# Performance work log

Hardware: AMD Instinct MI355X
Metric: run time of the kernel (lower is better)

## Reference

```python
import jax, jax.numpy as jnp
import numpy as np

N_EMBD = 512
NUM_HEADS = 8
HEAD_SIZE = 64


def setup_inputs() -> dict:
    key = jax.random.key(0)
    ks = jax.random.split(key, 6)
    B, T, C, H, D = 64, 256, N_EMBD, NUM_HEADS, HEAD_SIZE
    s = 0.02
    return {
        "x": jax.random.normal(ks[0], (B, T, C), dtype=jnp.float32),
        "wq": jax.random.normal(ks[1], (H, C, D), dtype=jnp.float32) * s,
        "wk": jax.random.normal(ks[2], (H, C, D), dtype=jnp.float32) * s,
        "wv": jax.random.normal(ks[3], (H, C, D), dtype=jnp.float32) * s,
        "bq": jnp.zeros((H, D), dtype=jnp.float32),
        "bk": jnp.zeros((H, D), dtype=jnp.float32),
        "bv": jnp.zeros((H, D), dtype=jnp.float32),
        "wo": jax.random.normal(ks[4], (H * D, C), dtype=jnp.float32) * s,
        "bo": jnp.zeros((C,), dtype=jnp.float32),
    }


def reference(x, wq, wk, wv, bq, bk, bv, wo, bo):
    B, T, C = x.shape
    H, _, D = wq.shape
    # per-head QKV projections (vectorized over heads)
    q = jnp.einsum('btc,hcd->bhtd', x, wq) + bq[None, :, None, :]
    k = jnp.einsum('btc,hcd->bhtd', x, wk) + bk[None, :, None, :]
    v = jnp.einsum('btc,hcd->bhtd', x, wv) + bv[None, :, None, :]
    scale = 1.0 / jnp.sqrt(jnp.asarray(D, dtype=x.dtype))
    scores = jnp.einsum('bhtd,bhsd->bhts', q, k) * scale  # [B,H,T,T]
    causal = jnp.tril(jnp.ones((T, T), dtype=bool))
    scores = jnp.where(causal[None, None], scores, -jnp.inf)
    weights = jax.nn.softmax(scores, axis=-1)  # dropout omitted (eval mode)
    out = jnp.einsum('bhts,bhsd->bhtd', weights, v)  # [B,H,T,D]
    combined = out.transpose(0, 2, 1, 3).reshape(B, T, H * D)
    return combined @ wo + bo
```

## Files before the change

kernel.cpp:

```cpp
#include <hip/hip_runtime.h>

typedef unsigned int   u32;
typedef unsigned short u16;
typedef __attribute__((ext_vector_type(8))) short short8;
typedef __attribute__((ext_vector_type(4))) float f32x4;


__device__ __forceinline__ u16 f2bf(float f) {
    u32 u = __float_as_uint(f);
    u += 0x7fffu + ((u >> 16) & 1u);
    return (u16)(u >> 16);
}

__device__ __forceinline__ void gload_lds16(const u16* g, u16* l) {
    __builtin_amdgcn_global_load_lds(
        (const __attribute__((address_space(1))) u32*)(const void*)g,
        (__attribute__((address_space(3))) u32*)(void*)l, 16, 0, 0);
}

__global__ void cast_x_kernel(const float* __restrict__ x, u16* __restrict__ xb) {
    int i = blockIdx.x * 256 + threadIdx.x;
    float4 v = ((const float4*)x)[i];
    ushort4 o;
    o.x = f2bf(v.x); o.y = f2bf(v.y); o.z = f2bf(v.z); o.w = f2bf(v.w);
    ((ushort4*)xb)[i] = o;
}

__global__ void pack_wqkv_kernel(const float* __restrict__ wq, const float* __restrict__ wk,
                                 const float* __restrict__ wv, u16* __restrict__ wt) {
    int i = blockIdx.x * 256 + threadIdx.x;
    int n = i >> 9, c = i & 511;
    int proj = n >> 9, hd = n & 511;
    int h = hd >> 6, d = hd & 63;
    const float* w = (proj == 0) ? wq : (proj == 1) ? wk : wv;
    wt[(size_t)n * 512 + c] = f2bf(w[h * 32768 + c * 64 + d]);
}

__global__ void pack_wo_kernel(const float* __restrict__ wo, u16* __restrict__ wt) {
    int i = blockIdx.x * 256 + threadIdx.x;
    int n = i >> 9, k = i & 511;
    wt[(size_t)n * 512 + k] = f2bf(wo[(size_t)k * 512 + n]);
}

template<int EPI, int NT>
__global__ __launch_bounds__(256)
void gemm128_kernel(const u16* __restrict__ A, const u16* __restrict__ Bt,
                    float* __restrict__ outf, const float* __restrict__ bo,
                    u16* __restrict__ Qb, u16* __restrict__ Kb, u16* __restrict__ Vb,
                    const float* __restrict__ bq, const float* __restrict__ bk,
                    const float* __restrict__ bv) {
    __shared__ __align__(16) u16 As[2][8192];
    __shared__ __align__(16) u16 Bs[2][8192];
    const int tid = threadIdx.x;
    const int bid = blockIdx.x;
    const int xcd = bid & 7;
    const int k8  = bid >> 3;
    const int m0 = (xcd * 16 + k8 / NT) * 128;
    const int n0 = (k8 % NT) * 128;
    const int w = tid >> 6, lane = tid & 63;
    const int srow = w * 8 + (lane >> 3);
    const int sc   = (lane & 7) ^ ((lane >> 3) & 7);
    const u16* Ag = A  + (size_t)(m0 + srow) * 512 + sc * 8;
    const u16* Bg = Bt + (size_t)(n0 + srow) * 512 + sc * 8;
    const int lofs = w * 512 + lane * 8;

    const int wrow = (w >> 1) * 64, wcol = (w & 1) * 64;
    const int lm = lane & 15, quad = lane >> 4;
    const int l7 = lm & 7;

    f32x4 acc[4][4] = {};

    #pragma unroll
    for (int j = 0; j < 4; ++j) {
        gload_lds16(Ag + j * (32 * 512), As[0] + j * 2048 + lofs);
        gload_lds16(Bg + j * (32 * 512), Bs[0] + j * 2048 + lofs);
    }

    #pragma unroll 1
    for (int kt = 0; kt < 8; ++kt) {
        __syncthreads();
        if (kt < 7) {
            const u16* Agp = Ag + (kt + 1) * 64;
            const u16* Bgp = Bg + (kt + 1) * 64;
            u16* Asp = As[(kt + 1) & 1] + lofs;
            u16* Bsp = Bs[(kt + 1) & 1] + lofs;
            #pragma unroll
            for (int j = 0; j < 4; ++j) {
                gload_lds16(Agp + j * (32 * 512), Asp + j * 2048);
                gload_lds16(Bgp + j * (32 * 512), Bsp + j * 2048);
            }
        }
        const u16* Ac = As[kt & 1];
        const u16* Bc = Bs[kt & 1];
        short8 af[2][4], bf[2][4];
        #pragma unroll
        for (int h = 0; h < 2; ++h) {
            const int slot = ((h * 4 + quad) ^ l7) * 8;
            #pragma unroll
            for (int mi = 0; mi < 4; ++mi)
                af[h][mi] = *(const short8*)(Ac + (wrow + mi * 16 + lm) * 64 + slot);
            #pragma unroll
            for (int ni = 0; ni < 4; ++ni)
                bf[h][ni] = *(const short8*)(Bc + (wcol + ni * 16 + lm) * 64 + slot);
        }
        #pragma unroll
        for (int h = 0; h < 2; ++h)
            #pragma unroll
            for (int mi = 0; mi < 4; ++mi)
                #pragma unroll
                for (int ni = 0; ni < 4; ++ni)
                    acc[mi][ni] = __builtin_amdgcn_mfma_f32_16x16x32_bf16(af[h][mi], bf[h][ni], acc[mi][ni], 0, 0, 0);
    }

    if (EPI == 1) {
        #pragma unroll
        for (int ni = 0; ni < 4; ++ni) {
            int ncol = n0 + wcol + ni * 16 + lm;
            float bias = bo[ncol];
            #pragma unroll
            for (int mi = 0; mi < 4; ++mi) {
                int mbase = m0 + wrow + mi * 16 + quad * 4;
                #pragma unroll
                for (int r = 0; r < 4; ++r)
                    outf[(size_t)(mbase + r) * 512 + ncol] = acc[mi][ni][r] + bias;
            }
        }
    } else {
        #pragma unroll
        for (int ni = 0; ni < 4; ++ni) {
            int ncol = n0 + wcol + ni * 16 + lm;
            int proj = ncol >> 9, hd = ncol & 511;
            int h = hd >> 6, d = hd & 63;
            const float* bptr = (proj == 0) ? bq : (proj == 1) ? bk : bv;
            u16* dst = (proj == 0) ? Qb : (proj == 1) ? Kb : Vb;
            float bias = bptr[hd];
            #pragma unroll
            for (int mi = 0; mi < 4; ++mi) {
                int mbase = m0 + wrow + mi * 16 + quad * 4;
                #pragma unroll
                for (int r = 0; r < 4; ++r) {
                    int mrow = mbase + r;
                    int b = mrow >> 8, t = mrow & 255;
                    size_t idx = (proj == 2)
                        ? ((size_t)((b * 8 + h) * 64 + d) * 256 + t)
                        : ((size_t)((b * 8 + h) * 256 + t) * 64 + d);
                    dst[idx] = f2bf(acc[mi][ni][r] + bias);
                }
            }
        }
    }
}

__global__ __launch_bounds__(256)
void attn_mfma_kernel(const u16* __restrict__ Qg, const u16* __restrict__ Kg,
                      const u16* __restrict__ Vtg, u16* __restrict__ attn) {
    __shared__ __align__(16) u16 lds[20480];
    const int bid = blockIdx.x;
    const int head = (bid & 7) * 64 + ((bid >> 3) >> 1);
    const int iset = (bid >> 3) & 1;
    const int b = head >> 3, h = head & 7;
    const int tid = threadIdx.x;
    const size_t hb = (size_t)head * 16384;

    {
        const uint4* Ksrc = (const uint4*)(Kg + hb);
        uint4* L4 = (uint4*)lds;
        #pragma unroll
        for (int it = 0; it < 8; ++it) {
            int g = it * 256 + tid;
            int kr = g >> 3, kc = g & 7;
            L4[kr * 8 + (kc ^ (kr & 7))] = Ksrc[g];
        }
    }
    __syncthreads();

    const int w = tid >> 6, lane = tid & 63;
    const int lm = lane & 15, quad = lane >> 4;
    const int l7 = lm & 7;

    const int kx0 = (quad ^ l7) * 8;
    const int kx1 = ((4 + quad) ^ l7) * 8;
    const u16* Kbase = lds + lm * 64;
    const u16* Vg = Vtg + hb;
    const int Pbase = 16384 + w * 1024;
    const int x0 = (lm >> 3) & 1;
    const int pw_even = Pbase + quad * 16 + l7 + x0 * 8;
    const int pw_odd  = Pbase + quad * 16 + l7 + (x0 ^ 1) * 8;
    const int pr0 = Pbase + ((lm & 3) * 4 + (quad >> 1)) * 64
                  + (2 * (lm >> 2) + ((quad & 1) ^ (lm & 1))) * 8;

    #pragma unroll 1
    for (int ii = 0; ii < 2; ++ii) {
        const int i = iset ? (ii ? 2 : 1) : (ii ? 3 : 0);
        const int t0 = i * 64 + w * 16;
        short8 qa0 = *(const short8*)(Qg + hb + (size_t)(t0 + lm) * 64 + quad * 8);
        short8 qa1 = *(const short8*)(Qg + hb + (size_t)(t0 + lm) * 64 + 32 + quad * 8);
        f32x4 O[4] = {};
        float mr[4] = {-INFINITY, -INFINITY, -INFINITY, -INFINITY};
        float lr[4] = {0.f, 0.f, 0.f, 0.f};

        #pragma unroll 1
        for (int j = 0; j <= i; ++j) {
            f32x4 S[4] = {};
            #pragma unroll
            for (int ni = 0; ni < 4; ++ni) {
                const u16* kp = Kbase + j * 4096 + ni * 1024;
                short8 kb0 = *(const short8*)(kp + kx0);
                short8 kb1 = *(const short8*)(kp + kx1);
                S[ni] = __builtin_amdgcn_mfma_f32_16x16x32_bf16(qa0, kb0, S[ni], 0, 0, 0);
                S[ni] = __builtin_amdgcn_mfma_f32_16x16x32_bf16(qa1, kb1, S[ni], 0, 0, 0);
            }
            short8 vb[4][2];
            #pragma unroll
            for (int nd = 0; nd < 4; ++nd) {
                const u16* vp = Vg + (size_t)(nd * 16 + lm) * 256 + j * 64;
                vb[nd][0] = *(const short8*)(vp + quad * 8);
                vb[nd][1] = *(const short8*)(vp + 32 + quad * 8);
            }
            if (j == i) {
                #pragma unroll
                for (int ni = 0; ni < 4; ++ni) {
                    int scol = ni * 16 + lm;
                    #pragma unroll
                    for (int rr = 0; rr < 4; ++rr) {
                        int tloc = w * 16 + quad * 4 + rr;
                        S[ni][rr] = (scol > tloc) ? -INFINITY : S[ni][rr] * 0.125f;
                    }
                }
            } else {
                #pragma unroll
                for (int ni = 0; ni < 4; ++ni)
                    #pragma unroll
                    for (int rr = 0; rr < 4; ++rr)
                        S[ni][rr] *= 0.125f;
            }
            float alpha[4];
            #pragma unroll
            for (int rr = 0; rr < 4; ++rr) {
                float mx = fmaxf(fmaxf(S[0][rr], S[1][rr]), fmaxf(S[2][rr], S[3][rr]));
                mx = fmaxf(mx, __shfl_xor(mx, 1));
                mx = fmaxf(mx, __shfl_xor(mx, 2));
                mx = fmaxf(mx, __shfl_xor(mx, 4));
                mx = fmaxf(mx, __shfl_xor(mx, 8));
                float mnew = fmaxf(mr[rr], mx);
                alpha[rr] = __expf(mr[rr] - mnew);
                mr[rr] = mnew;
            }
            float rs[4] = {0.f, 0.f, 0.f, 0.f};
            #pragma unroll
            for (int ni = 0; ni < 4; ++ni) {
                #pragma unroll
                for (int rr = 0; rr < 4; ++rr) {
                    float p = __expf(S[ni][rr] - mr[rr]);
                    rs[rr] += p;
                    int addr = ((rr & 1) ? pw_odd : pw_even) + (rr * 4 + ni) * 64;
                    lds[addr] = f2bf(p);
                }
            }
            #pragma unroll
            for (int rr = 0; rr < 4; ++rr) {
                float s = rs[rr];
                s += __shfl_xor(s, 1);
                s += __shfl_xor(s, 2);
                s += __shfl_xor(s, 4);
                s += __shfl_xor(s, 8);
                lr[rr] = lr[rr] * alpha[rr] + s;
                O[0][rr] *= alpha[rr]; O[1][rr] *= alpha[rr];
                O[2][rr] *= alpha[rr]; O[3][rr] *= alpha[rr];
            }
            __syncthreads();
            short8 pa0 = *(const short8*)(lds + pr0);
            short8 pa1 = *(const short8*)(lds + pr0 + 128);
            #pragma unroll
            for (int nd = 0; nd < 4; ++nd) {
                O[nd] = __builtin_amdgcn_mfma_f32_16x16x32_bf16(pa0, vb[nd][0], O[nd], 0, 0, 0);
                O[nd] = __builtin_amdgcn_mfma_f32_16x16x32_bf16(pa1, vb[nd][1], O[nd], 0, 0, 0);
            }
        }
        #pragma unroll
        for (int rr = 0; rr < 4; ++rr) {
            float inv = 1.0f / lr[rr];
            int t = t0 + quad * 4 + rr;
            u16* op = attn + (size_t)(b * 256 + t) * 512 + h * 64 + lm;
            op[0]  = f2bf(O[0][rr] * inv);
            op[16] = f2bf(O[1][rr] * inv);
            op[32] = f2bf(O[2][rr] * inv);
            op[48] = f2bf(O[3][rr] * inv);
        }
    }
}

extern "C" void kernel_launch(void* const* d_in, const int* in_sizes, int n_in,
                              void* d_out, int out_size, void* d_ws, size_t ws_size,
                              hipStream_t stream) {
    const float* x  = (const float*)d_in[0];
    const float* wq = (const float*)d_in[1];
    const float* wk = (const float*)d_in[2];
    const float* wv = (const float*)d_in[3];
    const float* bq = (const float*)d_in[4];
    const float* bk = (const float*)d_in[5];
    const float* bv = (const float*)d_in[6];
    const float* wo = (const float*)d_in[7];
    const float* bo = (const float*)d_in[8];
    float* out = (float*)d_out;

    char* ws = (char*)d_ws;
    const size_t SZ = 16777216;
    u16* xb    = (u16*)(ws);
    u16* Qb    = (u16*)(ws + SZ);
    u16* Kb    = (u16*)(ws + 2 * SZ);
    u16* Vt    = (u16*)(ws + 3 * SZ);
    u16* attn  = (u16*)(ws + 4 * SZ);
    u16* wqkvT = (u16*)(ws + 5 * SZ);
    u16* woT   = (u16*)(ws + 5 * SZ + 1572864);

    cast_x_kernel<<<8192, 256, 0, stream>>>(x, xb);
    pack_wqkv_kernel<<<3072, 256, 0, stream>>>(wq, wk, wv, wqkvT);
    pack_wo_kernel<<<1024, 256, 0, stream>>>(wo, woT);

    gemm128_kernel<0, 12><<<1536, 256, 0, stream>>>(
        xb, wqkvT, nullptr, nullptr, Qb, Kb, Vt, bq, bk, bv);

    attn_mfma_kernel<<<1024, 256, 0, stream>>>(Qb, Kb, Vt, attn);

    gemm128_kernel<1, 4><<<512, 256, 0, stream>>>(
        attn, woT, out, bo, nullptr, nullptr, nullptr, nullptr, nullptr, nullptr);
}
```

Baseline: 205.6 us.

## Use 512-thread GEMM blocks with triple-buffered LDS and vmcnt-based prefetch

Result: slower. 223.3 us (+8.6%).

```diff
diff --git a/kernel.cpp b/kernel.cpp
--- a/kernel.cpp
+++ b/kernel.cpp
@@ -43,14 +43,14 @@
 }
 
 template<int EPI, int NT>
-__global__ __launch_bounds__(256)
+__global__ __launch_bounds__(512)
 void gemm128_kernel(const u16* __restrict__ A, const u16* __restrict__ Bt,
                     float* __restrict__ outf, const float* __restrict__ bo,
                     u16* __restrict__ Qb, u16* __restrict__ Kb, u16* __restrict__ Vb,
                     const float* __restrict__ bq, const float* __restrict__ bk,
                     const float* __restrict__ bv) {
-    __shared__ __align__(16) u16 As[2][8192];
-    __shared__ __align__(16) u16 Bs[2][8192];
+    __shared__ __align__(16) u16 As[3][8192];
+    __shared__ __align__(16) u16 Bs[3][8192];
     const int tid = threadIdx.x;
     const int bid = blockIdx.x;
     const int xcd = bid & 7;
@@ -62,37 +62,41 @@
     const int sc   = (lane & 7) ^ ((lane >> 3) & 7);
     const u16* Ag = A  + (size_t)(m0 + srow) * 512 + sc * 8;
     const u16* Bg = Bt + (size_t)(n0 + srow) * 512 + sc * 8;
-    const int lofs = w * 512 + lane * 8;
-
-    const int wrow = (w >> 1) * 64, wcol = (w & 1) * 64;
+    const int lofs = tid * 8;
+
+    const int wrow = (w >> 2) * 64, wcol = (w & 3) * 32;
     const int lm = lane & 15, quad = lane >> 4;
     const int l7 = lm & 7;
 
-    f32x4 acc[4][4] = {};
-
-    #pragma unroll
-    for (int j = 0; j < 4; ++j) {
-        gload_lds16(Ag + j * (32 * 512), As[0] + j * 2048 + lofs);
-        gload_lds16(Bg + j * (32 * 512), Bs[0] + j * 2048 + lofs);
-    }
-
+    f32x4 acc[4][2] = {};
+
+#define STAGE(kt, b) do {                                        \
+        const u16* Agp = Ag + (kt) * 64;                         \
+        const u16* Bgp = Bg + (kt) * 64;                         \
+        u16* Asp = As[(b)] + lofs;                               \
+        u16* Bsp = Bs[(b)] + lofs;                               \
+        gload_lds16(Agp,            Asp);                        \
+        gload_lds16(Agp + 64 * 512, Asp + 4096);                 \
+        gload_lds16(Bgp,            Bsp);                        \
+        gload_lds16(Bgp + 64 * 512, Bsp + 4096);                 \
+    } while (0)
+
+    STAGE(0, 0);
+    STAGE(1, 1);
+
+    int cur = 0;
     #pragma unroll 1
     for (int kt = 0; kt < 8; ++kt) {
-        __syncthreads();
-        if (kt < 7) {
-            const u16* Agp = Ag + (kt + 1) * 64;
-            const u16* Bgp = Bg + (kt + 1) * 64;
-            u16* Asp = As[(kt + 1) & 1] + lofs;
-            u16* Bsp = Bs[(kt + 1) & 1] + lofs;
-            #pragma unroll
-            for (int j = 0; j < 4; ++j) {
-                gload_lds16(Agp + j * (32 * 512), Asp + j * 2048);
-                gload_lds16(Bgp + j * (32 * 512), Bsp + j * 2048);
-            }
-        }
-        const u16* Ac = As[kt & 1];
-        const u16* Bc = Bs[kt & 1];
-        short8 af[2][4], bf[2][4];
+        if (kt < 7) asm volatile("s_waitcnt vmcnt(4)" ::: "memory");
+        else        asm volatile("s_waitcnt vmcnt(0)" ::: "memory");
+        __builtin_amdgcn_s_barrier();
+        if (kt < 6) {
+            int sb = cur ? cur - 1 : 2;
+            STAGE(kt + 2, sb);
+        }
+        const u16* Ac = As[cur];
+        const u16* Bc = Bs[cur];
+        short8 af[2][4], bf[2][2];
         #pragma unroll
         for (int h = 0; h < 2; ++h) {
             const int slot = ((h * 4 + quad) ^ l7) * 8;
@@ -100,7 +104,7 @@
             for (int mi = 0; mi < 4; ++mi)
                 af[h][mi] = *(const short8*)(Ac + (wrow + mi * 16 + lm) * 64 + slot);
             #pragma unroll
-            for (int ni = 0; ni < 4; ++ni)
+            for (int ni = 0; ni < 2; ++ni)
                 bf[h][ni] = *(const short8*)(Bc + (wcol + ni * 16 + lm) * 64 + slot);
         }
         #pragma unroll
@@ -108,13 +112,15 @@
             #pragma unroll
             for (int mi = 0; mi < 4; ++mi)
                 #pragma unroll
-                for (int ni = 0; ni < 4; ++ni)
+                for (int ni = 0; ni < 2; ++ni)
                     acc[mi][ni] = __builtin_amdgcn_mfma_f32_16x16x32_bf16(af[h][mi], bf[h][ni], acc[mi][ni], 0, 0, 0);
+        cur = (cur == 2) ? 0 : cur + 1;
     }
+#undef STAGE
 
     if (EPI == 1) {
         #pragma unroll
-        for (int ni = 0; ni < 4; ++ni) {
+        for (int ni = 0; ni < 2; ++ni) {
             int ncol = n0 + wcol + ni * 16 + lm;
             float bias = bo[ncol];
             #pragma unroll
@@ -127,7 +133,7 @@
         }
     } else {
         #pragma unroll
-        for (int ni = 0; ni < 4; ++ni) {
+        for (int ni = 0; ni < 2; ++ni) {
             int ncol = n0 + wcol + ni * 16 + lm;
             int proj = ncol >> 9, hd = ncol & 511;
             int h = hd >> 6, d = hd & 63;
@@ -318,11 +324,11 @@
     pack_wqkv_kernel<<<3072, 256, 0, stream>>>(wq, wk, wv, wqkvT);
     pack_wo_kernel<<<1024, 256, 0, stream>>>(wo, woT);
 
-    gemm128_kernel<0, 12><<<1536, 256, 0, stream>>>(
+    gemm128_kernel<0, 12><<<1536, 512, 0, stream>>>(
         xb, wqkvT, nullptr, nullptr, Qb, Kb, Vt, bq, bk, bv);
 
     attn_mfma_kernel<<<1024, 256, 0, stream>>>(Qb, Kb, Vt, attn);
 
-    gemm128_kernel<1, 4><<<512, 256, 0, stream>>>(
+    gemm128_kernel<1, 4><<<512, 512, 0, stream>>>(
         attn, woT, out, bo, nullptr, nullptr, nullptr, nullptr, nullptr, nullptr);
 }
```

## Replace LDS-tiled GEMM with B-panel-resident kernel streaming A from global

Applied to the files above, without the earlier changes.

New measurement: 238.7 us. 1.16x slower.

```diff
diff --git a/kernel.cpp b/kernel.cpp
--- a/kernel.cpp
+++ b/kernel.cpp
@@ -43,70 +43,54 @@
 }
 
 template<int EPI, int NT>
-__global__ __launch_bounds__(256)
-void gemm128_kernel(const u16* __restrict__ A, const u16* __restrict__ Bt,
-                    float* __restrict__ outf, const float* __restrict__ bo,
-                    u16* __restrict__ Qb, u16* __restrict__ Kb, u16* __restrict__ Vb,
-                    const float* __restrict__ bq, const float* __restrict__ bk,
-                    const float* __restrict__ bv) {
-    __shared__ __align__(16) u16 As[2][8192];
-    __shared__ __align__(16) u16 Bs[2][8192];
+__global__ __launch_bounds__(1024)
+void gemm_bpanel_kernel(const u16* __restrict__ A, const u16* __restrict__ Bt,
+                        float* __restrict__ outf, const float* __restrict__ bo,
+                        u16* __restrict__ Qb, u16* __restrict__ Kb, u16* __restrict__ Vb,
+                        const float* __restrict__ bq, const float* __restrict__ bk,
+                        const float* __restrict__ bv) {
+    __shared__ __align__(16) u16 Bp[64 * 512];
     const int tid = threadIdx.x;
     const int bid = blockIdx.x;
     const int xcd = bid & 7;
-    const int k8  = bid >> 3;
-    const int m0 = (xcd * 16 + k8 / NT) * 128;
-    const int n0 = (k8 % NT) * 128;
+    const int idx = bid >> 3;
+    const int m0 = (xcd * 4 + idx / NT) * 512;
+    const int nt = idx % NT;
+    const int n0 = nt * 64;
     const int w = tid >> 6, lane = tid & 63;
-    const int srow = w * 8 + (lane >> 3);
-    const int sc   = (lane & 7) ^ ((lane >> 3) & 7);
-    const u16* Ag = A  + (size_t)(m0 + srow) * 512 + sc * 8;
-    const u16* Bg = Bt + (size_t)(n0 + srow) * 512 + sc * 8;
-    const int lofs = w * 512 + lane * 8;
-
-    const int wrow = (w >> 1) * 64, wcol = (w & 1) * 64;
+
+    {
+        const u16* src = Bt + (size_t)(n0 + lane) * 512;
+        #pragma unroll
+        for (int i = 0; i < 4; ++i) {
+            int kc = w * 4 + i;
+            gload_lds16(src + kc * 8, Bp + kc * 512 + lane * 8);
+        }
+    }
+    __syncthreads();
+
     const int lm = lane & 15, quad = lane >> 4;
-    const int l7 = lm & 7;
-
-    f32x4 acc[4][4] = {};
-
-    #pragma unroll
-    for (int j = 0; j < 4; ++j) {
-        gload_lds16(Ag + j * (32 * 512), As[0] + j * 2048 + lofs);
-        gload_lds16(Bg + j * (32 * 512), Bs[0] + j * 2048 + lofs);
-    }
-
-    #pragma unroll 1
+    const u16* Abase = A + (size_t)(m0 + w * 32 + lm) * 512 + quad * 8;
+    const u16* bfb = Bp + quad * 512 + lm * 8;
+
+    f32x4 acc[2][4] = {};
+
+    #pragma unroll 2
     for (int kt = 0; kt < 8; ++kt) {
-        __syncthreads();
-        if (kt < 7) {
-            const u16* Agp = Ag + (kt + 1) * 64;
-            const u16* Bgp = Bg + (kt + 1) * 64;
-            u16* Asp = As[(kt + 1) & 1] + lofs;
-            u16* Bsp = Bs[(kt + 1) & 1] + lofs;
-            #pragma unroll
-            for (int j = 0; j < 4; ++j) {
-                gload_lds16(Agp + j * (32 * 512), Asp + j * 2048);
-                gload_lds16(Bgp + j * (32 * 512), Bsp + j * 2048);
-            }
-        }
-        const u16* Ac = As[kt & 1];
-        const u16* Bc = Bs[kt & 1];
-        short8 af[2][4], bf[2][4];
+        short8 af[2][2], bf[2][4];
         #pragma unroll
         for (int h = 0; h < 2; ++h) {
-            const int slot = ((h * 4 + quad) ^ l7) * 8;
-            #pragma unroll
-            for (int mi = 0; mi < 4; ++mi)
-                af[h][mi] = *(const short8*)(Ac + (wrow + mi * 16 + lm) * 64 + slot);
+            #pragma unroll
+            for (int mi = 0; mi < 2; ++mi)
+                af[h][mi] = *(const short8*)(Abase + mi * 8192 + kt * 64 + h * 32);
             #pragma unroll
             for (int ni = 0; ni < 4; ++ni)
-                bf[h][ni] = *(const short8*)(Bc + (wcol + ni * 16 + lm) * 64 + slot);
+                bf[h][ni] = *(const short8*)(bfb + kt * 4096 + h * 2048 + ni * 128);
         }
         #pragma unroll
         for (int h = 0; h < 2; ++h)
             #pragma unroll
-            for (int mi = 0; mi < 4; ++mi)
+            for (int mi = 0; mi < 2; ++mi)
                 #pragma unroll
                 for (int ni = 0; ni < 4; ++ni)
                     acc[mi][ni] = __builtin_amdgcn_mfma_f32_16x16x32_bf16(af[h][mi], bf[h][ni], acc[mi][ni], 0, 0, 0);
@@ -115,36 +99,35 @@
     if (EPI == 1) {
         #pragma unroll
         for (int ni = 0; ni < 4; ++ni) {
-            int ncol = n0 + wcol + ni * 16 + lm;
+            int ncol = n0 + ni * 16 + lm;
             float bias = bo[ncol];
             #pragma unroll
-            for (int mi = 0; mi < 4; ++mi) {
-                int mbase = m0 + wrow + mi * 16 + quad * 4;
+            for (int mi = 0; mi < 2; ++mi) {
+                int rbase = m0 + w * 32 + mi * 16 + quad * 4;
                 #pragma unroll
                 for (int r = 0; r < 4; ++r)
-                    outf[(size_t)(mbase + r) * 512 + ncol] = acc[mi][ni][r] + bias;
+                    outf[(size_t)(rbase + r) * 512 + ncol] = acc[mi][ni][r] + bias;
             }
         }
     } else {
+        const int proj = nt >> 3, hh = nt & 7;
+        const float* bptr = (proj == 0) ? bq : (proj == 1) ? bk : bv;
+        u16* dst = (proj == 0) ? Qb : (proj == 1) ? Kb : Vb;
         #pragma unroll
         for (int ni = 0; ni < 4; ++ni) {
-            int ncol = n0 + wcol + ni * 16 + lm;
-            int proj = ncol >> 9, hd = ncol & 511;
-            int h = hd >> 6, d = hd & 63;
-            const float* bptr = (proj == 0) ? bq : (proj == 1) ? bk : bv;
-            u16* dst = (proj == 0) ? Qb : (proj == 1) ? Kb : Vb;
-            float bias = bptr[hd];
-            #pragma unroll
-            for (int mi = 0; mi < 4; ++mi) {
-                int mbase = m0 + wrow + mi * 16 + quad * 4;
+            int d = ni * 16 + lm;
+            float bias = bptr[hh * 64 + d];
+            #pragma unroll
+            for (int mi = 0; mi < 2; ++mi) {
+                int rbase = m0 + w * 32 + mi * 16 + quad * 4;
                 #pragma unroll
                 for (int r = 0; r < 4; ++r) {
-                    int mrow = mbase + r;
-                    int b = mrow >> 8, t = mrow & 255;
-                    size_t idx = (proj == 2)
-                        ? ((size_t)((b * 8 + h) * 64 + d) * 256 + t)
-                        : ((size_t)((b * 8 + h) * 256 + t) * 64 + d);
-                    dst[idx] = f2bf(acc[mi][ni][r] + bias);
+                    int row = rbase + r;
+                    int b = row >> 8, t = row & 255;
+                    size_t idxo = (proj == 2)
+                        ? ((size_t)((b * 8 + hh) * 64 + d) * 256 + t)
+                        : ((size_t)((b * 8 + hh) * 256 + t) * 64 + d);
+                    dst[idxo] = f2bf(acc[mi][ni][r] + bias);
                 }
             }
         }
@@ -318,11 +301,11 @@
     pack_wqkv_kernel<<<3072, 256, 0, stream>>>(wq, wk, wv, wqkvT);
     pack_wo_kernel<<<1024, 256, 0, stream>>>(wo, woT);
 
-    gemm128_kernel<0, 12><<<1536, 256, 0, stream>>>(
+    gemm_bpanel_kernel<0, 24><<<768, 1024, 0, stream>>>(
         xb, wqkvT, nullptr, nullptr, Qb, Kb, Vt, bq, bk, bv);
 
     attn_mfma_kernel<<<1024, 256, 0, stream>>>(Qb, Kb, Vt, attn);
 
-    gemm128_kernel<1, 4><<<512, 256, 0, stream>>>(
+    gemm_bpanel_kernel<1, 8><<<256, 1024, 0, stream>>>(
         attn, woT, out, bo, nullptr, nullptr, nullptr, nullptr, nullptr, nullptr);
 }
```

## Load GEMM B operand directly from global, halve LDS, vectorize V-transpose stores

Applied to the files above, without the earlier changes.

New measurement: 222.6 us. 1.08x slower.

```diff
diff --git a/kernel.cpp b/kernel.cpp
--- a/kernel.cpp
+++ b/kernel.cpp
@@ -43,14 +43,13 @@
 }
 
 template<int EPI, int NT>
-__global__ __launch_bounds__(256)
+__global__ __launch_bounds__(256, 4)
 void gemm128_kernel(const u16* __restrict__ A, const u16* __restrict__ Bt,
                     float* __restrict__ outf, const float* __restrict__ bo,
                     u16* __restrict__ Qb, u16* __restrict__ Kb, u16* __restrict__ Vb,
                     const float* __restrict__ bq, const float* __restrict__ bk,
                     const float* __restrict__ bv) {
     __shared__ __align__(16) u16 As[2][8192];
-    __shared__ __align__(16) u16 Bs[2][8192];
     const int tid = threadIdx.x;
     const int bid = blockIdx.x;
     const int xcd = bid & 7;
@@ -60,57 +59,51 @@
     const int w = tid >> 6, lane = tid & 63;
     const int srow = w * 8 + (lane >> 3);
     const int sc   = (lane & 7) ^ ((lane >> 3) & 7);
-    const u16* Ag = A  + (size_t)(m0 + srow) * 512 + sc * 8;
-    const u16* Bg = Bt + (size_t)(n0 + srow) * 512 + sc * 8;
+    const u16* Ag = A + (size_t)(m0 + srow) * 512 + sc * 8;
     const int lofs = w * 512 + lane * 8;
 
     const int wrow = (w >> 1) * 64, wcol = (w & 1) * 64;
     const int lm = lane & 15, quad = lane >> 4;
     const int l7 = lm & 7;
 
+    const u16* Bg0 = Bt + (size_t)(n0 + wcol + lm) * 512 + quad * 8;
+
     f32x4 acc[4][4] = {};
 
-    #pragma unroll
-    for (int j = 0; j < 4; ++j) {
-        gload_lds16(Ag + j * (32 * 512), As[0] + j * 2048 + lofs);
-        gload_lds16(Bg + j * (32 * 512), Bs[0] + j * 2048 + lofs);
-    }
+#define STAGE_A(kt, b) do {                                      \
+        const u16* Agp = Ag + (kt) * 64;                         \
+        u16* Asp = As[(b)] + lofs;                               \
+        gload_lds16(Agp,             Asp);                       \
+        gload_lds16(Agp + 32 * 512,  Asp + 2048);                \
+        gload_lds16(Agp + 64 * 512,  Asp + 4096);                \
+        gload_lds16(Agp + 96 * 512,  Asp + 6144);                \
+    } while (0)
+
+    STAGE_A(0, 0);
 
     #pragma unroll 1
     for (int kt = 0; kt < 8; ++kt) {
         __syncthreads();
-        if (kt < 7) {
-            const u16* Agp = Ag + (kt + 1) * 64;
-            const u16* Bgp = Bg + (kt + 1) * 64;
-            u16* Asp = As[(kt + 1) & 1] + lofs;
-            u16* Bsp = Bs[(kt + 1) & 1] + lofs;
-            #pragma unroll
-            for (int j = 0; j < 4; ++j) {
-                gload_lds16(Agp + j * (32 * 512), Asp + j * 2048);
-                gload_lds16(Bgp + j * (32 * 512), Bsp + j * 2048);
-            }
-        }
+        if (kt < 7) STAGE_A(kt + 1, (kt + 1) & 1);
         const u16* Ac = As[kt & 1];
-        const u16* Bc = Bs[kt & 1];
-        short8 af[2][4], bf[2][4];
         #pragma unroll
         for (int h = 0; h < 2; ++h) {
             const int slot = ((h * 4 + quad) ^ l7) * 8;
+            short8 af[4], bf[4];
             #pragma unroll
             for (int mi = 0; mi < 4; ++mi)
-                af[h][mi] = *(const short8*)(Ac + (wrow + mi * 16 + lm) * 64 + slot);
+                af[mi] = *(const short8*)(Ac + (wrow + mi * 16 + lm) * 64 + slot);
             #pragma unroll
             for (int ni = 0; ni < 4; ++ni)
-                bf[h][ni] = *(const short8*)(Bc + (wcol + ni * 16 + lm) * 64 + slot);
-        }
-        #pragma unroll
-        for (int h = 0; h < 2; ++h)
+                bf[ni] = *(const short8*)(Bg0 + (size_t)(ni * 16) * 512 + kt * 64 + h * 32);
             #pragma unroll
             for (int mi = 0; mi < 4; ++mi)
                 #pragma unroll
                 for (int ni = 0; ni < 4; ++ni)
-                    acc[mi][ni] = __builtin_amdgcn_mfma_f32_16x16x32_bf16(af[h][mi], bf[h][ni], acc[mi][ni], 0, 0, 0);
+                    acc[mi][ni] = __builtin_amdgcn_mfma_f32_16x16x32_bf16(af[mi], bf[ni], acc[mi][ni], 0, 0, 0);
+        }
     }
+#undef STAGE_A
 
     if (EPI == 1) {
         #pragma unroll
@@ -137,14 +130,22 @@
             #pragma unroll
             for (int mi = 0; mi < 4; ++mi) {
                 int mbase = m0 + wrow + mi * 16 + quad * 4;
-                #pragma unroll
-                for (int r = 0; r < 4; ++r) {
-                    int mrow = mbase + r;
-                    int b = mrow >> 8, t = mrow & 255;
-                    size_t idx = (proj == 2)
-                        ? ((size_t)((b * 8 + h) * 64 + d) * 256 + t)
-                        : ((size_t)((b * 8 + h) * 256 + t) * 64 + d);
-                    dst[idx] = f2bf(acc[mi][ni][r] + bias);
+                if (proj == 2) {
+                    int b = mbase >> 8, t = mbase & 255;
+                    ushort4 v4;
+                    v4.x = f2bf(acc[mi][ni][0] + bias);
+                    v4.y = f2bf(acc[mi][ni][1] + bias);
+                    v4.z = f2bf(acc[mi][ni][2] + bias);
+                    v4.w = f2bf(acc[mi][ni][3] + bias);
+                    *(ushort4*)(dst + ((size_t)((b * 8 + h) * 64 + d) * 256 + t)) = v4;
+                } else {
+                    #pragma unroll
+                    for (int r = 0; r < 4; ++r) {
+                        int mrow = mbase + r;
+                        int b = mrow >> 8, t = mrow & 255;
+                        dst[(size_t)((b * 8 + h) * 256 + t) * 64 + d] =
+                            f2bf(acc[mi][ni][r] + bias);
+                    }
                 }
             }
         }
```
